# Kernel tuning notes

Measured on AMD Instinct MI355X. Metric: run time of the kernel, lower is better.

Reference implementation:

```python
import jax, jax.numpy as jnp
import numpy as np

N, IN, OUT, H = 4096, 512, 64, 8
ALPHA = 0.2
NEG = -9e15


def glorot(key, shape):
    fan_in, fan_out = shape[-2], shape[-1]
    limit = np.sqrt(6.0 / (fan_in + fan_out))
    return jax.random.uniform(key, shape, jnp.float32, -limit, limit)


def setup_inputs() -> dict:
    key = jax.random.key(0)
    k1, k2, k3, k4, k5 = jax.random.split(key, 5)
    x = jax.random.normal(k1, (N, IN), jnp.float32)
    adj = jax.random.randint(k2, (N, N), 0, 2, jnp.int32)
    W = glorot(k3, (H, IN, OUT))            # stacked per-head kernels
    a1 = glorot(k4, (H, OUT, 1))[..., 0]    # [H, OUT] self attn vec
    a2 = glorot(k5, (H, OUT, 1))[..., 0]    # [H, OUT] neigh attn vec
    return {"x": x, "adj": adj, "W": W, "a1": a1, "a2": a2}


def reference(x, adj, W, a1, a2):
    # Wh: [H, N, OUT]
    Wh = jnp.einsum("ni,hio->hno", x, W)
    f1 = jnp.einsum("hno,ho->hn", Wh, a1)  # [H, N]
    f2 = jnp.einsum("hno,ho->hn", Wh, a2)  # [H, N]
    e = jax.nn.leaky_relu(f1[:, :, None] + f2[:, None, :], ALPHA)  # [H, N, N]
    e = jnp.where(adj[None] > 0, e, NEG)
    attn = jax.nn.softmax(e, axis=-1)       # dropout inactive (eval mode)
    h = jnp.einsum("hnm,hmo->hno", attn, Wh)  # [H, N, OUT]
    # concat heads along features -> [N, H*OUT]
    out = jnp.transpose(h, (1, 0, 2)).reshape(N, H * OUT)
    return out
```

## Files before the change

kernel.cpp:

```cpp
#include <hip/hip_runtime.h>
#include <hip/hip_bf16.h>
#include <stdint.h>


constexpr int N_ = 4096, IN_ = 512, OUT_ = 64, H_ = 8;
constexpr float ALPHA_ = 0.2f;

typedef __attribute__((ext_vector_type(8))) short short8;
typedef __attribute__((ext_vector_type(4))) float f32x4;

__device__ __forceinline__ uint32_t rne_pack2(float a, float b, float& ra, float& rb) {
    uint32_t ua = __float_as_uint(a); ua += 0x7fffu + ((ua >> 16) & 1u); ua >>= 16;
    uint32_t ub = __float_as_uint(b); ub += 0x7fffu + ((ub >> 16) & 1u); ub >>= 16;
    ra = __uint_as_float(ua << 16);
    rb = __uint_as_float(ub << 16);
    return ua | (ub << 16);
}

__global__ __launch_bounds__(256) void pack_adj(const int* __restrict__ adj,
                                                unsigned long long* __restrict__ bitsT) {
    size_t g = (size_t)blockIdx.x * 256 + threadIdx.x;
    int v = adj[g];
    unsigned long long m = __ballot(v != 0);
    if ((threadIdx.x & 63) == 0) {
        int n = (int)(g >> 12);
        int c = (int)((g >> 6) & 63);
        bitsT[(size_t)c * N_ + n] = m;
    }
}

__global__ __launch_bounds__(256) void split_x(const float* __restrict__ x,
                                               uint16_t* __restrict__ xh,
                                               uint16_t* __restrict__ xl) {
    size_t g = ((size_t)blockIdx.x * 256 + threadIdx.x) * 8;
    float4 v0 = *(const float4*)(x + g);
    float4 v1 = *(const float4*)(x + g + 4);
    float v[8] = {v0.x, v0.y, v0.z, v0.w, v1.x, v1.y, v1.z, v1.w};
    uint32_t ph[4], pl[4];
#pragma unroll
    for (int i = 0; i < 4; i++) {
        float h0, h1, d0, d1;
        ph[i] = rne_pack2(v[2 * i], v[2 * i + 1], h0, h1);
        pl[i] = rne_pack2(v[2 * i] - h0, v[2 * i + 1] - h1, d0, d1);
    }
    *(uint4*)(xh + g) = make_uint4(ph[0], ph[1], ph[2], ph[3]);
    *(uint4*)(xl + g) = make_uint4(pl[0], pl[1], pl[2], pl[3]);
}

__global__ __launch_bounds__(256) void split_wT(const float* __restrict__ W,
                                                uint16_t* __restrict__ WTh,
                                                uint16_t* __restrict__ WTl) {
    __shared__ float T[64 * 68];
    const int t  = threadIdx.x;
    const int kb = blockIdx.x;
    const int h  = blockIdx.y;
    {
        int kk = t >> 2, os = (t & 3) * 16;
        const float* src = W + ((size_t)h * IN_ + kb * 64 + kk) * OUT_ + os;
#pragma unroll
        for (int j = 0; j < 4; j++)
            *(float4*)&T[kk * 68 + os + j * 4] = *(const float4*)(src + j * 4);
    }
    __syncthreads();
    int o = t >> 2, ks = (t & 3) * 16;
    uint32_t ph[8], pl[8];
#pragma unroll
    for (int i = 0; i < 8; i++) {
        float va = T[(ks + 2 * i) * 68 + o], vb = T[(ks + 2 * i + 1) * 68 + o];
        float h0, h1, d0, d1;
        ph[i] = rne_pack2(va, vb, h0, h1);
        pl[i] = rne_pack2(va - h0, vb - h1, d0, d1);
    }
    size_t dst = ((size_t)h * OUT_ + o) * IN_ + kb * 64 + ks;
    *(uint4*)&WTh[dst]     = make_uint4(ph[0], ph[1], ph[2], ph[3]);
    *(uint4*)&WTh[dst + 8] = make_uint4(ph[4], ph[5], ph[6], ph[7]);
    *(uint4*)&WTl[dst]     = make_uint4(pl[0], pl[1], pl[2], pl[3]);
    *(uint4*)&WTl[dst + 8] = make_uint4(pl[4], pl[5], pl[6], pl[7]);
}

__global__ __launch_bounds__(256) void wh_mfma(const uint16_t* __restrict__ xh,
                                               const uint16_t* __restrict__ xl,
                                               const uint16_t* __restrict__ WTh,
                                               const uint16_t* __restrict__ WTl,
                                               const float* __restrict__ a1,
                                               const float* __restrict__ a2,
                                               uint16_t* __restrict__ WhhT,
                                               float* __restrict__ f1,
                                               float* __restrict__ f2) {
    __shared__ __align__(16) char ldsbuf[4 * 64 * 72 * 2];
    uint16_t* Ah = (uint16_t*)ldsbuf;
    uint16_t* Al = Ah + 64 * 72;
    uint16_t* Bh = Al + 64 * 72;
    uint16_t* Bl = Bh + 64 * 72;
    const int t  = threadIdx.x;
    const int h  = blockIdx.y;
    const int n0 = blockIdx.x * 64;
    const int l  = t & 63, w = t >> 6;
    const int p  = l & 15, q = l >> 4;
    const int sr = t >> 2, sc = (t & 3) * 16;

    f32x4 acc[4];
#pragma unroll
    for (int rt = 0; rt < 4; rt++) acc[rt] = (f32x4){0.f, 0.f, 0.f, 0.f};

    const uint16_t* gxh = xh + (size_t)(n0 + sr) * IN_ + sc;
    const uint16_t* gxl = xl + (size_t)(n0 + sr) * IN_ + sc;
    const uint16_t* gbh = WTh + ((size_t)h * OUT_ + sr) * IN_ + sc;
    const uint16_t* gbl = WTl + ((size_t)h * OUT_ + sr) * IN_ + sc;

    for (int kt = 0; kt < 8; kt++) {
        __syncthreads();
        uint4 a0 = *(const uint4*)(gxh + kt * 64);
        uint4 a1v = *(const uint4*)(gxh + kt * 64 + 8);
        uint4 b0 = *(const uint4*)(gxl + kt * 64);
        uint4 b1 = *(const uint4*)(gxl + kt * 64 + 8);
        uint4 c0 = *(const uint4*)(gbh + kt * 64);
        uint4 c1 = *(const uint4*)(gbh + kt * 64 + 8);
        uint4 d0 = *(const uint4*)(gbl + kt * 64);
        uint4 d1 = *(const uint4*)(gbl + kt * 64 + 8);
        *(uint4*)&Ah[sr * 72 + sc]     = a0;
        *(uint4*)&Ah[sr * 72 + sc + 8] = a1v;
        *(uint4*)&Al[sr * 72 + sc]     = b0;
        *(uint4*)&Al[sr * 72 + sc + 8] = b1;
        *(uint4*)&Bh[sr * 72 + sc]     = c0;
        *(uint4*)&Bh[sr * 72 + sc + 8] = c1;
        *(uint4*)&Bl[sr * 72 + sc]     = d0;
        *(uint4*)&Bl[sr * 72 + sc + 8] = d1;
        __syncthreads();
#pragma unroll
        for (int k0 = 0; k0 < 2; k0++) {
            short8 bhf = *(const short8*)&Bh[(w * 16 + p) * 72 + q * 8 + k0 * 32];
            short8 blf = *(const short8*)&Bl[(w * 16 + p) * 72 + q * 8 + k0 * 32];
#pragma unroll
            for (int rt = 0; rt < 4; rt++) {
                short8 ahf = *(const short8*)&Ah[(rt * 16 + p) * 72 + q * 8 + k0 * 32];
                short8 alf = *(const short8*)&Al[(rt * 16 + p) * 72 + q * 8 + k0 * 32];
                acc[rt] = __builtin_amdgcn_mfma_f32_16x16x32_bf16(ahf, bhf, acc[rt], 0, 0, 0);
                acc[rt] = __builtin_amdgcn_mfma_f32_16x16x32_bf16(alf, bhf, acc[rt], 0, 0, 0);
                acc[rt] = __builtin_amdgcn_mfma_f32_16x16x32_bf16(ahf, blf, acc[rt], 0, 0, 0);
            }
        }
    }
    __syncthreads();
    float* Whs = (float*)ldsbuf;
#pragma unroll
    for (int rt = 0; rt < 4; rt++)
#pragma unroll
        for (int reg = 0; reg < 4; reg++)
            Whs[(rt * 16 + q * 4 + reg) * 68 + w * 16 + p] = acc[rt][reg];
    __syncthreads();
    {
        int r = t >> 2, og = (t & 3) * 16;
        float s1 = 0.f, s2 = 0.f;
#pragma unroll
        for (int j = 0; j < 4; j++) {
            float4 wv = *(const float4*)&Whs[r * 68 + og + j * 4];
            float4 av = *(const float4*)(a1 + h * OUT_ + og + j * 4);
            float4 bv = *(const float4*)(a2 + h * OUT_ + og + j * 4);
            s1 += wv.x * av.x + wv.y * av.y + wv.z * av.z + wv.w * av.w;
            s2 += wv.x * bv.x + wv.y * bv.y + wv.z * bv.z + wv.w * bv.w;
        }
        s1 += __shfl_xor(s1, 1, 64); s1 += __shfl_xor(s1, 2, 64);
        s2 += __shfl_xor(s2, 1, 64); s2 += __shfl_xor(s2, 2, 64);
        if ((t & 3) == 0) {
            f1[(size_t)h * N_ + n0 + r] = s1;
            f2[(size_t)h * N_ + n0 + r] = s2;
        }
    }
    {
        int o = t >> 2, ns = (t & 3) * 16;
        uint32_t ph[8];
#pragma unroll
        for (int i = 0; i < 8; i++) {
            float va = Whs[(ns + 2 * i) * 68 + o], vb = Whs[(ns + 2 * i + 1) * 68 + o];
            float h0, h1;
            ph[i] = rne_pack2(va, vb, h0, h1);
        }
        size_t dst = ((size_t)h * OUT_ + o) * N_ + n0 + ns;
        *(uint4*)&WhhT[dst]     = make_uint4(ph[0], ph[1], ph[2], ph[3]);
        *(uint4*)&WhhT[dst + 8] = make_uint4(ph[4], ph[5], ph[6], ph[7]);
    }
}

__global__ __launch_bounds__(256, 4) void gat_main(const unsigned long long* __restrict__ bitsT,
                                                   const uint16_t* __restrict__ WhhT,
                                                   const float* __restrict__ f1,
                                                   const float* __restrict__ f2,
                                                   float* __restrict__ outNum,
                                                   float* __restrict__ op1,
                                                   float* __restrict__ Lpart) {
    __shared__ __align__(16) uint16_t Bh[64 * 72];
    const int t  = threadIdx.x;
    const int h  = blockIdx.y, z = blockIdx.z;
    const int n0 = blockIdx.x * 64;
    const int l  = t & 63, w = t >> 6;
    const int p  = l & 15, q = l >> 4;
    const int sr = t >> 2, sc = (t & 3) * 16;
    const int row = w * 16 + p;

    const float f1v = f1[(size_t)h * N_ + n0 + row];
    const float* f2b = f2 + (size_t)h * N_;
    const uint16_t* gb = WhhT + ((size_t)h * OUT_ + sr) * N_ + sc;

    float Lp = 0.f;
    f32x4 acc[4];
#pragma unroll
    for (int ct = 0; ct < 4; ct++) acc[ct] = (f32x4){0.f, 0.f, 0.f, 0.f};

    for (int cc = 0; cc < 32; cc++) {
        const int chunk = z * 32 + cc;
        const int m0 = chunk * 64;
        __syncthreads();
        uint4 b0 = *(const uint4*)(gb + m0);
        uint4 b1 = *(const uint4*)(gb + m0 + 8);
        *(uint4*)&Bh[sr * 72 + sc]     = b0;
        *(uint4*)&Bh[sr * 72 + sc + 8] = b1;
        unsigned long long word = bitsT[(size_t)chunk * N_ + n0 + row];
        __syncthreads();
#pragma unroll
        for (int k0 = 0; k0 < 2; k0++) {
            const float* fp = f2b + m0 + k0 * 32 + q * 8;
            float4 fv0 = *(const float4*)fp;
            float4 fv1 = *(const float4*)(fp + 4);
            float fs[8] = {fv0.x, fv0.y, fv0.z, fv0.w, fv1.x, fv1.y, fv1.z, fv1.w};
            uint32_t bits8 = (uint32_t)(word >> (k0 * 32 + q * 8)) & 0xffu;
            float pv[8];
#pragma unroll
            for (int j = 0; j < 8; j++) {
                float s = f1v + fs[j];
                float e = fmaxf(s, ALPHA_ * s);
                float ex = __expf(e);
                pv[j] = ((bits8 >> j) & 1u) ? ex : 0.f;
            }
            union { short8 s8; uint32_t u[4]; } af;
#pragma unroll
            for (int i = 0; i < 4; i++) {
                float r0, r1;
                af.u[i] = rne_pack2(pv[2 * i], pv[2 * i + 1], r0, r1);
                Lp += r0 + r1;
            }
#pragma unroll
            for (int ct = 0; ct < 4; ct++) {
                short8 bhf = *(const short8*)&Bh[(ct * 16 + p) * 72 + q * 8 + k0 * 32];
                acc[ct] = __builtin_amdgcn_mfma_f32_16x16x32_bf16(af.s8, bhf, acc[ct], 0, 0, 0);
            }
        }
    }
    float Ls = Lp;
    Ls += __shfl_xor(Ls, 16, 64);
    Ls += __shfl_xor(Ls, 32, 64);
    if (q == 0) Lpart[((size_t)z * 8 + h) * N_ + n0 + row] = Ls;
    float* dst = (z == 0) ? outNum : op1;
#pragma unroll
    for (int ct = 0; ct < 4; ct++)
#pragma unroll
        for (int reg = 0; reg < 4; reg++) {
            int rr = w * 16 + q * 4 + reg;
            dst[(size_t)(n0 + rr) * (H_ * OUT_) + h * OUT_ + ct * 16 + p] = acc[ct][reg];
        }
}

__global__ __launch_bounds__(256) void combine(float* __restrict__ outb,
                                               const float* __restrict__ op1,
                                               const float* __restrict__ Lpart) {
    size_t g = (size_t)blockIdx.x * 256 + threadIdx.x;
    int n = (int)(g >> 7);
    int c = (int)(g & 127);
    int h = c >> 4;
    float4 o0 = ((const float4*)outb)[g];
    float4 o1 = ((const float4*)op1)[g];
    float L = Lpart[(size_t)h * N_ + n] + Lpart[(size_t)(8 + h) * N_ + n];
    float inv = 1.f / L;
    ((float4*)outb)[g] = make_float4((o0.x + o1.x) * inv, (o0.y + o1.y) * inv,
                                     (o0.z + o1.z) * inv, (o0.w + o1.w) * inv);
}

extern "C" void kernel_launch(void* const* d_in, const int* in_sizes, int n_in,
                              void* d_out, int out_size, void* d_ws, size_t ws_size,
                              hipStream_t stream) {
    const float* x   = nullptr;
    const int*   adj = nullptr;
    const float* W   = nullptr;
    const float* a1  = nullptr;
    const float* a2  = nullptr;
    for (int i = 0; i < n_in; i++) {
        long long sz = in_sizes[i];
        if      (sz == (long long)N_ * IN_)        x   = (const float*)d_in[i];
        else if (sz == (long long)N_ * N_)         adj = (const int*)d_in[i];
        else if (sz == (long long)H_ * IN_ * OUT_) W   = (const float*)d_in[i];
        else if (sz == (long long)H_ * OUT_) {
            if (!a1) a1 = (const float*)d_in[i];
            else     a2 = (const float*)d_in[i];
        }
    }
    if (!x)   x   = (const float*)d_in[0];
    if (!adj) adj = (const int*)d_in[1];
    if (!W)   W   = (const float*)d_in[2];
    if (!a1)  a1  = (const float*)d_in[3];
    if (!a2)  a2  = (const float*)d_in[4];
    float* out = (float*)d_out;

    char* ws = (char*)d_ws;
    unsigned long long* bitsT = (unsigned long long*)ws;
    uint16_t* WhhT = (uint16_t*)(ws + (2u  << 20));
    float* f1      = (float*)   (ws + (6u  << 20));
    float* f2      = (float*)   (ws + (6u  << 20) + (128u << 10));
    float* Lpart   = (float*)   (ws + (6u  << 20) + (256u << 10));
    float* op1     = (float*)   (ws + (6u  << 20) + (512u << 10));
    uint16_t* xh   = (uint16_t*)(ws + (6u  << 20) + (512u << 10));
    uint16_t* xl   = (uint16_t*)(ws + (10u << 20) + (512u << 10));
    uint16_t* WTh  = (uint16_t*)(ws + (14u << 20) + (512u << 10));
    uint16_t* WTl  = (uint16_t*)(ws + (15u << 20));

    pack_adj<<<(N_ * (size_t)N_) / 256, 256, 0, stream>>>(adj, bitsT);
    split_x<<<(N_ * IN_) / (256 * 8), 256, 0, stream>>>(x, xh, xl);
    split_wT<<<dim3(IN_ / 64, H_), 256, 0, stream>>>(W, WTh, WTl);
    wh_mfma<<<dim3(N_ / 64, H_), 256, 0, stream>>>(xh, xl, WTh, WTl, a1, a2, WhhT, f1, f2);
    gat_main<<<dim3(N_ / 64, H_, 2), 256, 0, stream>>>(bitsT, WhhT, f1, f2, out, op1, Lpart);
    combine<<<(N_ * H_ * OUT_) / (256 * 4), 256, 0, stream>>>(out, op1, Lpart);
}
```

Baseline: 212.7 us.

## Fuse x splitting into Wh GEMM, drop LDS staging and split-K combine

The x hi/lo bf16 split moves inside the Wh MFMA kernel, which removes the split_x launch and its intermediate buffers. Both GEMM kernels now load MFMA fragments straight from global memory instead of staging tiles in LDS with barriers. The attention kernel no longer splits the neighbour dimension in two, so the op1/Lpart partials and the combine kernel go away. The softmax denominator is now computed by an extra MFMA against a ones vector, and the output is normalised in the epilogue. In exchange, grid parallelism in gat_main is halved, and global fragment loads may be less coalesced than the LDS-staged ones.

```diff
diff --git a/kernel.cpp b/kernel.cpp
--- a/kernel.cpp
+++ b/kernel.cpp
@@ -9,12 +9,22 @@
 typedef __attribute__((ext_vector_type(8))) short short8;
 typedef __attribute__((ext_vector_type(4))) float f32x4;
 
+__device__ __forceinline__ uint32_t pkbf(float a, float b) {
+    union { __hip_bfloat162 h2; uint32_t u; } c;
+    c.h2 = __float22bfloat162_rn(make_float2(a, b));
+    return c.u;
+}
 __device__ __forceinline__ uint32_t rne_pack2(float a, float b, float& ra, float& rb) {
     uint32_t ua = __float_as_uint(a); ua += 0x7fffu + ((ua >> 16) & 1u); ua >>= 16;
     uint32_t ub = __float_as_uint(b); ub += 0x7fffu + ((ub >> 16) & 1u); ub >>= 16;
     ra = __uint_as_float(ua << 16);
     rb = __uint_as_float(ub << 16);
     return ua | (ub << 16);
+}
+__device__ __forceinline__ short8 ld_bf8(const uint16_t* ptr) {
+    union { uint4 v; short8 s; } u;
+    u.v = *(const uint4*)ptr;
+    return u.s;
 }
 
 __global__ __launch_bounds__(256) void pack_adj(const int* __restrict__ adj,
@@ -29,24 +39,6 @@
     }
 }
 
-__global__ __launch_bounds__(256) void split_x(const float* __restrict__ x,
-                                               uint16_t* __restrict__ xh,
-                                               uint16_t* __restrict__ xl) {
-    size_t g = ((size_t)blockIdx.x * 256 + threadIdx.x) * 8;
-    float4 v0 = *(const float4*)(x + g);
-    float4 v1 = *(const float4*)(x + g + 4);
-    float v[8] = {v0.x, v0.y, v0.z, v0.w, v1.x, v1.y, v1.z, v1.w};
-    uint32_t ph[4], pl[4];
-#pragma unroll
-    for (int i = 0; i < 4; i++) {
-        float h0, h1, d0, d1;
-        ph[i] = rne_pack2(v[2 * i], v[2 * i + 1], h0, h1);
-        pl[i] = rne_pack2(v[2 * i] - h0, v[2 * i + 1] - h1, d0, d1);
-    }
-    *(uint4*)(xh + g) = make_uint4(ph[0], ph[1], ph[2], ph[3]);
-    *(uint4*)(xl + g) = make_uint4(pl[0], pl[1], pl[2], pl[3]);
-}
-
 __global__ __launch_bounds__(256) void split_wT(const float* __restrict__ W,
                                                 uint16_t* __restrict__ WTh,
                                                 uint16_t* __restrict__ WTl) {
@@ -78,8 +70,7 @@
     *(uint4*)&WTl[dst + 8] = make_uint4(pl[4], pl[5], pl[6], pl[7]);
 }
 
-__global__ __launch_bounds__(256) void wh_mfma(const uint16_t* __restrict__ xh,
-                                               const uint16_t* __restrict__ xl,
+__global__ __launch_bounds__(256) void wh_mfma(const float* __restrict__ x,
                                                const uint16_t* __restrict__ WTh,
                                                const uint16_t* __restrict__ WTl,
                                                const float* __restrict__ a1,
@@ -87,67 +78,53 @@
                                                uint16_t* __restrict__ WhhT,
                                                float* __restrict__ f1,
                                                float* __restrict__ f2) {
-    __shared__ __align__(16) char ldsbuf[4 * 64 * 72 * 2];
-    uint16_t* Ah = (uint16_t*)ldsbuf;
-    uint16_t* Al = Ah + 64 * 72;
-    uint16_t* Bh = Al + 64 * 72;
-    uint16_t* Bl = Bh + 64 * 72;
-    const int t  = threadIdx.x;
-    const int h  = blockIdx.y;
-    const int n0 = blockIdx.x * 64;
-    const int l  = t & 63, w = t >> 6;
-    const int p  = l & 15, q = l >> 4;
-    const int sr = t >> 2, sc = (t & 3) * 16;
+    __shared__ __align__(16) float Whs[64 * 68];
+    const int t = threadIdx.x, h = blockIdx.y, n0 = blockIdx.x * 64;
+    const int l = t & 63, w = t >> 6, p = l & 15, q = l >> 4;
 
     f32x4 acc[4];
 #pragma unroll
-    for (int rt = 0; rt < 4; rt++) acc[rt] = (f32x4){0.f, 0.f, 0.f, 0.f};
-
-    const uint16_t* gxh = xh + (size_t)(n0 + sr) * IN_ + sc;
-    const uint16_t* gxl = xl + (size_t)(n0 + sr) * IN_ + sc;
-    const uint16_t* gbh = WTh + ((size_t)h * OUT_ + sr) * IN_ + sc;
-    const uint16_t* gbl = WTl + ((size_t)h * OUT_ + sr) * IN_ + sc;
+    for (int ct = 0; ct < 4; ct++) acc[ct] = (f32x4){0.f, 0.f, 0.f, 0.f};
+
+    const float* gx = x + (size_t)(n0 + w * 16 + p) * IN_ + q * 8;
+    const uint16_t* gbh[4];
+    const uint16_t* gbl[4];
+#pragma unroll
+    for (int ct = 0; ct < 4; ct++) {
+        gbh[ct] = WTh + ((size_t)h * OUT_ + ct * 16 + p) * IN_ + q * 8;
+        gbl[ct] = WTl + ((size_t)h * OUT_ + ct * 16 + p) * IN_ + q * 8;
+    }
 
     for (int kt = 0; kt < 8; kt++) {
-        __syncthreads();
-        uint4 a0 = *(const uint4*)(gxh + kt * 64);
-        uint4 a1v = *(const uint4*)(gxh + kt * 64 + 8);
-        uint4 b0 = *(const uint4*)(gxl + kt * 64);
-        uint4 b1 = *(const uint4*)(gxl + kt * 64 + 8);
-        uint4 c0 = *(const uint4*)(gbh + kt * 64);
-        uint4 c1 = *(const uint4*)(gbh + kt * 64 + 8);
-        uint4 d0 = *(const uint4*)(gbl + kt * 64);
-        uint4 d1 = *(const uint4*)(gbl + kt * 64 + 8);
-        *(uint4*)&Ah[sr * 72 + sc]     = a0;
-        *(uint4*)&Ah[sr * 72 + sc + 8] = a1v;
-        *(uint4*)&Al[sr * 72 + sc]     = b0;
-        *(uint4*)&Al[sr * 72 + sc + 8] = b1;
-        *(uint4*)&Bh[sr * 72 + sc]     = c0;
-        *(uint4*)&Bh[sr * 72 + sc + 8] = c1;
-        *(uint4*)&Bl[sr * 72 + sc]     = d0;
-        *(uint4*)&Bl[sr * 72 + sc + 8] = d1;
-        __syncthreads();
 #pragma unroll
         for (int k0 = 0; k0 < 2; k0++) {
-            short8 bhf = *(const short8*)&Bh[(w * 16 + p) * 72 + q * 8 + k0 * 32];
-            short8 blf = *(const short8*)&Bl[(w * 16 + p) * 72 + q * 8 + k0 * 32];
-#pragma unroll
-            for (int rt = 0; rt < 4; rt++) {
-                short8 ahf = *(const short8*)&Ah[(rt * 16 + p) * 72 + q * 8 + k0 * 32];
-                short8 alf = *(const short8*)&Al[(rt * 16 + p) * 72 + q * 8 + k0 * 32];
-                acc[rt] = __builtin_amdgcn_mfma_f32_16x16x32_bf16(ahf, bhf, acc[rt], 0, 0, 0);
-                acc[rt] = __builtin_amdgcn_mfma_f32_16x16x32_bf16(alf, bhf, acc[rt], 0, 0, 0);
-                acc[rt] = __builtin_amdgcn_mfma_f32_16x16x32_bf16(ahf, blf, acc[rt], 0, 0, 0);
+            const int off = kt * 64 + k0 * 32;
+            float4 xa = *(const float4*)(gx + off);
+            float4 xb = *(const float4*)(gx + off + 4);
+            float va[8] = {xa.x, xa.y, xa.z, xa.w, xb.x, xb.y, xb.z, xb.w};
+            union { short8 s; uint32_t u[4]; } ah, al;
+#pragma unroll
+            for (int i = 0; i < 4; i++) {
+                ah.u[i] = pkbf(va[2 * i], va[2 * i + 1]);
+                float ha = __uint_as_float(ah.u[i] << 16);
+                float hb = __uint_as_float(ah.u[i] & 0xffff0000u);
+                al.u[i] = pkbf(va[2 * i] - ha, va[2 * i + 1] - hb);
             }
-        }
-    }
-    __syncthreads();
-    float* Whs = (float*)ldsbuf;
-#pragma unroll
-    for (int rt = 0; rt < 4; rt++)
+#pragma unroll
+            for (int ct = 0; ct < 4; ct++) {
+                short8 bh = ld_bf8(gbh[ct] + off);
+                short8 bl = ld_bf8(gbl[ct] + off);
+                acc[ct] = __builtin_amdgcn_mfma_f32_16x16x32_bf16(ah.s, bh, acc[ct], 0, 0, 0);
+                acc[ct] = __builtin_amdgcn_mfma_f32_16x16x32_bf16(al.s, bh, acc[ct], 0, 0, 0);
+                acc[ct] = __builtin_amdgcn_mfma_f32_16x16x32_bf16(ah.s, bl, acc[ct], 0, 0, 0);
+            }
+        }
+    }
+#pragma unroll
+    for (int ct = 0; ct < 4; ct++)
 #pragma unroll
         for (int reg = 0; reg < 4; reg++)
-            Whs[(rt * 16 + q * 4 + reg) * 68 + w * 16 + p] = acc[rt][reg];
+            Whs[(w * 16 + q * 4 + reg) * 68 + ct * 16 + p] = acc[ct][reg];
     __syncthreads();
     {
         int r = t >> 2, og = (t & 3) * 16;
@@ -182,97 +159,77 @@
     }
 }
 
-__global__ __launch_bounds__(256, 4) void gat_main(const unsigned long long* __restrict__ bitsT,
-                                                   const uint16_t* __restrict__ WhhT,
-                                                   const float* __restrict__ f1,
-                                                   const float* __restrict__ f2,
-                                                   float* __restrict__ outNum,
-                                                   float* __restrict__ op1,
-                                                   float* __restrict__ Lpart) {
-    __shared__ __align__(16) uint16_t Bh[64 * 72];
-    const int t  = threadIdx.x;
-    const int h  = blockIdx.y, z = blockIdx.z;
-    const int n0 = blockIdx.x * 64;
-    const int l  = t & 63, w = t >> 6;
-    const int p  = l & 15, q = l >> 4;
-    const int sr = t >> 2, sc = (t & 3) * 16;
+__global__ __launch_bounds__(256) void gat_main(const unsigned long long* __restrict__ bitsT,
+                                                const uint16_t* __restrict__ WhhT,
+                                                const float* __restrict__ f1,
+                                                const float* __restrict__ f2,
+                                                float* __restrict__ out) {
+    const int t = threadIdx.x, h = blockIdx.y, n0 = blockIdx.x * 64;
+    const int l = t & 63, w = t >> 6, p = l & 15, q = l >> 4;
     const int row = w * 16 + p;
 
     const float f1v = f1[(size_t)h * N_ + n0 + row];
-    const float* f2b = f2 + (size_t)h * N_;
-    const uint16_t* gb = WhhT + ((size_t)h * OUT_ + sr) * N_ + sc;
-
-    float Lp = 0.f;
-    f32x4 acc[4];
+    const float* f2b = f2 + (size_t)h * N_ + q * 8;
+    const unsigned long long* bp = bitsT + n0 + row;
+    const uint16_t* gb[4];
+#pragma unroll
+    for (int ct = 0; ct < 4; ct++)
+        gb[ct] = WhhT + ((size_t)h * OUT_ + ct * 16 + p) * N_ + q * 8;
+
+    short8 ones;
+    {
+        union { short8 s; uint32_t u[4]; } o;
+        o.u[0] = o.u[1] = o.u[2] = o.u[3] = 0x3f803f80u;
+        ones = o.s;
+    }
+
+    f32x4 acc[4], accL;
 #pragma unroll
     for (int ct = 0; ct < 4; ct++) acc[ct] = (f32x4){0.f, 0.f, 0.f, 0.f};
-
-    for (int cc = 0; cc < 32; cc++) {
-        const int chunk = z * 32 + cc;
+    accL = (f32x4){0.f, 0.f, 0.f, 0.f};
+
+    for (int chunk = 0; chunk < 64; chunk++) {
         const int m0 = chunk * 64;
-        __syncthreads();
-        uint4 b0 = *(const uint4*)(gb + m0);
-        uint4 b1 = *(const uint4*)(gb + m0 + 8);
-        *(uint4*)&Bh[sr * 72 + sc]     = b0;
-        *(uint4*)&Bh[sr * 72 + sc + 8] = b1;
-        unsigned long long word = bitsT[(size_t)chunk * N_ + n0 + row];
-        __syncthreads();
+        unsigned long long word = bp[(size_t)chunk * N_];
 #pragma unroll
         for (int k0 = 0; k0 < 2; k0++) {
-            const float* fp = f2b + m0 + k0 * 32 + q * 8;
-            float4 fv0 = *(const float4*)fp;
-            float4 fv1 = *(const float4*)(fp + 4);
+            const int off = m0 + k0 * 32;
+            short8 b0 = ld_bf8(gb[0] + off);
+            short8 b1 = ld_bf8(gb[1] + off);
+            short8 b2 = ld_bf8(gb[2] + off);
+            short8 b3 = ld_bf8(gb[3] + off);
+            float4 fv0 = *(const float4*)(f2b + off);
+            float4 fv1 = *(const float4*)(f2b + off + 4);
             float fs[8] = {fv0.x, fv0.y, fv0.z, fv0.w, fv1.x, fv1.y, fv1.z, fv1.w};
             uint32_t bits8 = (uint32_t)(word >> (k0 * 32 + q * 8)) & 0xffu;
-            float pv[8];
-#pragma unroll
-            for (int j = 0; j < 8; j++) {
-                float s = f1v + fs[j];
-                float e = fmaxf(s, ALPHA_ * s);
-                float ex = __expf(e);
-                pv[j] = ((bits8 >> j) & 1u) ? ex : 0.f;
+            union { short8 s; uint32_t u[4]; } af;
+#pragma unroll
+            for (int i = 0; i < 4; i++) {
+                float s0 = f1v + fs[2 * i];
+                float s1 = f1v + fs[2 * i + 1];
+                float e0 = fmaxf(s0, ALPHA_ * s0);
+                float e1 = fmaxf(s1, ALPHA_ * s1);
+                float x0 = ((bits8 >> (2 * i)) & 1u) ? __expf(e0) : 0.f;
+                float x1 = ((bits8 >> (2 * i + 1)) & 1u) ? __expf(e1) : 0.f;
+                af.u[i] = pkbf(x0, x1);
             }
-            union { short8 s8; uint32_t u[4]; } af;
-#pragma unroll
-            for (int i = 0; i < 4; i++) {
-                float r0, r1;
-                af.u[i] = rne_pack2(pv[2 * i], pv[2 * i + 1], r0, r1);
-                Lp += r0 + r1;
-            }
-#pragma unroll
-            for (int ct = 0; ct < 4; ct++) {
-                short8 bhf = *(const short8*)&Bh[(ct * 16 + p) * 72 + q * 8 + k0 * 32];
-                acc[ct] = __builtin_amdgcn_mfma_f32_16x16x32_bf16(af.s8, bhf, acc[ct], 0, 0, 0);
-            }
-        }
-    }
-    float Ls = Lp;
-    Ls += __shfl_xor(Ls, 16, 64);
-    Ls += __shfl_xor(Ls, 32, 64);
-    if (q == 0) Lpart[((size_t)z * 8 + h) * N_ + n0 + row] = Ls;
-    float* dst = (z == 0) ? outNum : op1;
+            accL   = __builtin_amdgcn_mfma_f32_16x16x32_bf16(af.s, ones, accL, 0, 0, 0);
+            acc[0] = __builtin_amdgcn_mfma_f32_16x16x32_bf16(af.s, b0, acc[0], 0, 0, 0);
+            acc[1] = __builtin_amdgcn_mfma_f32_16x16x32_bf16(af.s, b1, acc[1], 0, 0, 0);
+            acc[2] = __builtin_amdgcn_mfma_f32_16x16x32_bf16(af.s, b2, acc[2], 0, 0, 0);
+            acc[3] = __builtin_amdgcn_mfma_f32_16x16x32_bf16(af.s, b3, acc[3], 0, 0, 0);
+        }
+    }
+    float invL[4];
+#pragma unroll
+    for (int reg = 0; reg < 4; reg++) invL[reg] = 1.0f / accL[reg];
 #pragma unroll
     for (int ct = 0; ct < 4; ct++)
 #pragma unroll
         for (int reg = 0; reg < 4; reg++) {
             int rr = w * 16 + q * 4 + reg;
-            dst[(size_t)(n0 + rr) * (H_ * OUT_) + h * OUT_ + ct * 16 + p] = acc[ct][reg];
-        }
-}
-
-__global__ __launch_bounds__(256) void combine(float* __restrict__ outb,
-                                               const float* __restrict__ op1,
-                                               const float* __restrict__ Lpart) {
-    size_t g = (size_t)blockIdx.x * 256 + threadIdx.x;
-    int n = (int)(g >> 7);
-    int c = (int)(g & 127);
-    int h = c >> 4;
-    float4 o0 = ((const float4*)outb)[g];
-    float4 o1 = ((const float4*)op1)[g];
-    float L = Lpart[(size_t)h * N_ + n] + Lpart[(size_t)(8 + h) * N_ + n];
-    float inv = 1.f / L;
-    ((float4*)outb)[g] = make_float4((o0.x + o1.x) * inv, (o0.y + o1.y) * inv,
-                                     (o0.z + o1.z) * inv, (o0.w + o1.w) * inv);
+            out[(size_t)(n0 + rr) * (H_ * OUT_) + h * OUT_ + ct * 16 + p] = acc[ct][reg] * invL[reg];
+        }
 }
 
 extern "C" void kernel_launch(void* const* d_in, const int* in_sizes, int n_in,
@@ -302,20 +259,14 @@
 
     char* ws = (char*)d_ws;
     unsigned long long* bitsT = (unsigned long long*)ws;
-    uint16_t* WhhT = (uint16_t*)(ws + (2u  << 20));
-    float* f1      = (float*)   (ws + (6u  << 20));
-    float* f2      = (float*)   (ws + (6u  << 20) + (128u << 10));
-    float* Lpart   = (float*)   (ws + (6u  << 20) + (256u << 10));
-    float* op1     = (float*)   (ws + (6u  << 20) + (512u << 10));
-    uint16_t* xh   = (uint16_t*)(ws + (6u  << 20) + (512u << 10));
-    uint16_t* xl   = (uint16_t*)(ws + (10u << 20) + (512u << 10));
-    uint16_t* WTh  = (uint16_t*)(ws + (14u << 20) + (512u << 10));
-    uint16_t* WTl  = (uint16_t*)(ws + (15u << 20));
+    uint16_t* WhhT = (uint16_t*)(ws + (2u << 20));
+    float* f1      = (float*)   (ws + (6u << 20));
+    float* f2      = (float*)   (ws + (6u << 20) + (128u << 10));
+    uint16_t* WTh  = (uint16_t*)(ws + (6u << 20) + (512u << 10));
+    uint16_t* WTl  = (uint16_t*)(ws + (7u << 20));
 
     pack_adj<<<(N_ * (size_t)N_) / 256, 256, 0, stream>>>(adj, bitsT);
-    split_x<<<(N_ * IN_) / (256 * 8), 256, 0, stream>>>(x, xh, xl);
     split_wT<<<dim3(IN_ / 64, H_), 256, 0, stream>>>(W, WTh, WTl);
-    wh_mfma<<<dim3(N_ / 64, H_), 256, 0, stream>>>(xh, xl, WTh, WTl, a1, a2, WhhT, f1, f2);
-    gat_main<<<dim3(N_ / 64, H_, 2), 256, 0, stream>>>(bitsT, WhhT, f1, f2, out, op1, Lpart);
-    combine<<<(N_ * H_ * OUT_) / (256 * 4), 256, 0, stream>>>(out, op1, Lpart);
-}
+    wh_mfma<<<dim3(N_ / 64, H_), 256, 0, stream>>>(x, WTh, WTl, a1, a2, WhhT, f1, f2);
+    gat_main<<<dim3(N_ / 64, H_), 256, 0, stream>>>(bitsT, WhhT, f1, f2, out);
+}
```

After: 290.4 us. 36.6% more time.
